# Kernel tuning notes

Measured on AMD Instinct MI355X. Metric: run time of the kernel, lower is better.

Reference implementation:

```python
import jax, jax.numpy as jnp
import numpy as np

B, K, D, LS, NL = 32, 64, 256, 128, 2


def _xavier(key, shape):
    # torch xavier_uniform for Linear weight [out, in]
    fan_out, fan_in = shape[-2], shape[-1]
    lim = float(np.sqrt(6.0 / (fan_in + fan_out)))
    return jax.random.uniform(key, shape, jnp.float32, -lim, lim)


def setup_inputs():
    key = jax.random.key(0)
    ks = jax.random.split(key, 32)
    inp = {
        "X": jax.random.normal(ks[0], (B, K, D), jnp.float32),
        # per-layer stacked params [NL, ...]
        "k_w": _xavier(ks[1], (NL, D, D)),
        "q_w": _xavier(ks[2], (NL, D, D)),
        "rv_w1": _xavier(ks[3], (NL, D, 2 * D)),
        "rv_b1": jnp.zeros((NL, D), jnp.float32),
        "rv_w2": _xavier(ks[4], (NL, D, D)),
        "rv_b2": jnp.zeros((NL, D), jnp.float32),
        "ln_g": jnp.ones((NL, D), jnp.float32),
        "ln_b": jnp.zeros((NL, D), jnp.float32),
        "mlp_w1": _xavier(ks[5], (NL, D, D)),
        "mlp_b1": jnp.zeros((NL, D), jnp.float32),
        "mlp_w2": _xavier(ks[6], (NL, D, D)),
        "mlp_b2": jnp.zeros((NL, D), jnp.float32),
        "proj_w": _xavier(ks[7], (LS, D)),
        "proj_b": jnp.zeros((LS,), jnp.float32),
        "mu_w": _xavier(ks[8], (LS, LS)),
        "mu_b": jnp.zeros((LS,), jnp.float32),
        "sp_w": _xavier(ks[9], (LS, LS)),
        "sp_b": jnp.zeros((LS,), jnp.float32),
    }
    return inp


def _gelu(x):
    return jax.nn.gelu(x, approximate=False)


def _layernorm(x, g, b, eps=1e-5):
    m = jnp.mean(x, axis=-1, keepdims=True)
    v = jnp.mean((x - m) ** 2, axis=-1, keepdims=True)
    return (x - m) / jnp.sqrt(v + eps) * g + b


def _block(x, kw, qw, rw1, rb1, rw2, rb2, lg, lb, mw1, mb1, mw2, mb2):
    scale = D ** (-0.5)
    x_orig = x
    # pairwise difference r[b,i,j,:] = x[b,i]-x[b,j]
    r = x[:, :, None, :] - x[:, None, :, :]                      # [B,K,K,D]
    xi = jnp.broadcast_to(x[:, :, None, :], (B, K, K, D))
    cat = jnp.concatenate([xi, r], axis=-1)                      # [B,K,K,2D]
    v = _gelu(jnp.einsum('bijc,dc->bijd', cat, rw1) + rb1)
    v = jnp.einsum('bijd,ed->bije', v, rw2) + rb2                # [B,K,K,D]
    k = jnp.einsum('bid,ed->bie', x, kw)
    q = jnp.einsum('bid,ed->bie', x, qw) * scale
    attn = jax.nn.softmax(jnp.einsum('bid,bjd->bij', q, k), axis=2)
    agg = jnp.einsum('bij,bijd->bid', attn, v)
    h = _layernorm(x_orig + agg, lg, lb)
    h = jnp.einsum('bid,ed->bie', _gelu(jnp.einsum('bid,ed->bie', h, mw1) + mb1), mw2) + mb2
    return x_orig + h


def reference(X, k_w, q_w, rv_w1, rv_b1, rv_w2, rv_b2, ln_g, ln_b,
              mlp_w1, mlp_b1, mlp_w2, mlp_b2, proj_w, proj_b,
              mu_w, mu_b, sp_w, sp_b):
    x = X
    for i in range(NL):
        x = _block(x, k_w[i], q_w[i], rv_w1[i], rv_b1[i], rv_w2[i], rv_b2[i],
                   ln_g[i], ln_b[i], mlp_w1[i], mlp_b1[i], mlp_w2[i], mlp_b2[i])
    s = jnp.sum(x, axis=1)                                        # [B,D]
    h = _gelu(s @ proj_w.T + proj_b)                              # [B,LS]
    mu = h @ mu_w.T + mu_b
    scale = jax.nn.softplus(h @ sp_w.T + sp_b)
    return (mu, scale)
```

## Files before the change

### kernel.cpp

```cpp
#include <hip/hip_runtime.h>
#include <hip/hip_bf16.h>

#define NL 2

using bf16 = __hip_bfloat16;
typedef short bf16x8 __attribute__((ext_vector_type(8)));
typedef float f32x4 __attribute__((ext_vector_type(4)));

__device__ __forceinline__ float bfu(unsigned short u) { return __uint_as_float(((unsigned)u) << 16); }

__device__ __forceinline__ unsigned short bfr(float v) {
  unsigned u = __float_as_uint(v);
  u += 0x7FFFu + ((u >> 16) & 1u);
  return (unsigned short)(u >> 16);
}

__device__ __forceinline__ float gelu_s(float x) {
  float e = __expf(-1.702f * x);
  return x * __builtin_amdgcn_rcpf(1.0f + e);
}

__device__ __forceinline__ float gelu_e(float x) {
  return 0.5f * x * (1.0f + erff(x * 0.7071067811865475f));
}

__device__ __forceinline__ float load_f(const void* p, int i, int fl) {
  if (fl) return bfu(((const unsigned short*)p)[i]);
  return ((const float*)p)[i];
}

__device__ __forceinline__ int block_detect(const void* X) {
  __shared__ int bad_s;
  if (threadIdx.x == 0) bad_s = 0;
  __syncthreads();
  if (threadIdx.x < 256) {
    const float v = bfu(((const unsigned short*)X)[threadIdx.x]);
    if (!(fabsf(v) < 1e6f)) atomicOr(&bad_s, 1);
  }
  __syncthreads();
  return bad_s ? 0 : 1;
}

__device__ __forceinline__ void stage_split4(unsigned short (&aF)[2][4096], int row, int d0, float4 v) {
  ushort4 h, lo;
  h.x = bfr(v.x); h.y = bfr(v.y); h.z = bfr(v.z); h.w = bfr(v.w);
  lo.x = bfr(v.x - bfu(h.x)); lo.y = bfr(v.y - bfu(h.y));
  lo.z = bfr(v.z - bfu(h.z)); lo.w = bfr(v.w - bfu(h.w));
  const int kt = d0 >> 5, lane = row | (((d0 >> 3) & 3) << 4), j = d0 & 7;
  *(ushort4*)&aF[0][kt*512 + lane*8 + j] = h;
  *(ushort4*)&aF[1][kt*512 + lane*8 + j] = lo;
}

__global__ __launch_bounds__(256) void prep_kernel(
    const void* __restrict__ X, const void* __restrict__ kw, const void* __restrict__ qw,
    const void* __restrict__ rw1, const void* __restrict__ rw2, const void* __restrict__ mw1,
    const void* __restrict__ mw2, const void* __restrict__ pw, const void* __restrict__ muw,
    const void* __restrict__ spw,
    const void* __restrict__ rb1, const void* __restrict__ rb2, const void* __restrict__ lng,
    const void* __restrict__ lnb, const void* __restrict__ mb1, const void* __restrict__ mb2,
    const void* __restrict__ pb, const void* __restrict__ mub, const void* __restrict__ spb,
    unsigned short* __restrict__ wfb, unsigned short* __restrict__ w3b,
    float* __restrict__ wh, float* __restrict__ bc)
{
  __shared__ __align__(16) char psm[65536];
  const int fl = block_detect(X);
  const int t = threadIdx.x;
  int blk = blockIdx.x;

  if (blk < 16) {
    unsigned short* ls = (unsigned short*)psm;
    unsigned* lsu = (unsigned*)psm;
    const int l = blk >> 3, kt = blk & 7;
    if (fl) {
      #pragma unroll
      for (int s = 0; s < 4; ++s) {
        const unsigned* sp = (const unsigned*)((s == 0) ? kw : (s == 1) ? qw : rw1);
        const int rstr = (s < 2) ? 128 : 256;
        const int coff = ((s == 3) ? 128 : 0) + kt*16;
        for (int i = t; i < 4096; i += 256) {
          const int e = i >> 4, d2 = i & 15;
          lsu[s*4096 + i] = sp[(l*256 + e)*rstr + coff + d2];
        }
      }
    } else {
      #pragma unroll
      for (int s = 0; s < 4; ++s) {
        const float* sp = (const float*)((s == 0) ? kw : (s == 1) ? qw : rw1);
        const int rstr = (s < 2) ? 256 : 512;
        const int coff = ((s == 3) ? 256 : 0) + kt*32;
        for (int i = t; i < 4096; i += 256) {
          const int e = i >> 4, d2 = i & 15;
          const float f0 = sp[(l*256 + e)*rstr + coff + d2*2];
          const float f1 = sp[(l*256 + e)*rstr + coff + d2*2 + 1];
          lsu[s*4096 + i] = (unsigned)bfr(f0) | ((unsigned)bfr(f1) << 16);
        }
      }
    }
    __syncthreads();
    unsigned* outp = (unsigned*)wfb + (l*8 + kt)*16384;
    for (int f2 = t; f2 < 16384; f2 += 256) {
      const int j2 = f2 & 3, lane = (f2 >> 2) & 63, ntg = f2 >> 8;
      const int seg = ntg >> 4;
      const int e = (ntg & 15)*16 + (lane & 15);
      const int dl = ((lane >> 4) & 3)*8 + j2*2;
      unsigned short r0 = ls[seg*8192 + e*32 + dl];
      unsigned short r1 = ls[seg*8192 + e*32 + dl + 1];
      if (seg == 1) { r0 = bfr(bfu(r0)*0.0625f); r1 = bfr(bfu(r1)*0.0625f); }
      else if (seg == 2) {
        const unsigned short w0 = ls[3*8192 + e*32 + dl];
        const unsigned short w1 = ls[3*8192 + e*32 + dl + 1];
        r0 = bfr(bfu(r0) + bfu(w0)); r1 = bfr(bfu(r1) + bfu(w1));
      }
      outp[f2] = (unsigned)r0 | ((unsigned)r1 << 16);
    }
    return;
  }
  blk -= 16;
  if (blk < 48) {
    unsigned short* ls = (unsigned short*)psm;
    unsigned* lsu = (unsigned*)psm;
    const int l3 = blk >> 3, kt = blk & 7;
    const int l = l3 / 3, gm = l3 % 3;
    const void* src = (gm == 0) ? rw2 : (gm == 1) ? mw1 : mw2;
    if (fl) {
      const unsigned* sp = (const unsigned*)src;
      for (int i = t; i < 4096; i += 256) {
        const int e = i >> 4, d2 = i & 15;
        lsu[i] = sp[(l*256 + e)*128 + kt*16 + d2];
      }
    } else {
      const float* sp = (const float*)src;
      for (int i = t; i < 4096; i += 256) {
        const int e = i >> 4, d2 = i & 15;
        const float f0 = sp[(l*256 + e)*256 + kt*32 + d2*2];
        const float f1 = sp[(l*256 + e)*256 + kt*32 + d2*2 + 1];
        lsu[i] = (unsigned)bfr(f0) | ((unsigned)bfr(f1) << 16);
      }
    }
    __syncthreads();
    unsigned* outp = (unsigned*)w3b + (l3*8 + kt)*4096;
    for (int f2 = t; f2 < 4096; f2 += 256) {
      const int j2 = f2 & 3, lane = (f2 >> 2) & 63, nt = f2 >> 8;
      const int e = nt*16 + (lane & 15);
      const int dl = ((lane >> 4) & 3)*8 + j2*2;
      outp[f2] = (unsigned)ls[e*32 + dl] | ((unsigned)ls[e*32 + dl + 1] << 16);
    }
    return;
  }
  blk -= 48;
  if (blk < 24) {
    float* lsf = (float*)psm;
    if (blk < 8) {
      const int l0 = blk*16;
      if (fl) {
        const unsigned* sp = (const unsigned*)pw;
        for (int i = t; i < 2048; i += 256) {
          const int ll = i >> 7, d2 = i & 127;
          const unsigned u = sp[(l0 + ll)*128 + d2];
          lsf[ll*256 + d2*2]     = __uint_as_float(u << 16);
          lsf[ll*256 + d2*2 + 1] = __uint_as_float(u & 0xffff0000u);
        }
      } else {
        const float* sp = (const float*)pw;
        for (int i = t; i < 4096; i += 256) {
          const int ll = i >> 8, d = i & 255;
          lsf[ll*256 + d] = sp[(l0 + ll)*256 + d];
        }
      }
      __syncthreads();
      for (int i = t; i < 4096; i += 256) {
        const int d = i >> 4, ll = i & 15;
        wh[d*128 + l0 + ll] = lsf[ll*256 + d];
      }
    } else {
      const int grp = blk - 8;
      const int isSp = grp >> 3;
      const int l0 = (grp & 7)*16;
      const void* src = isSp ? spw : muw;
      const int off = isSp ? 49152 : 32768;
      if (fl) {
        const unsigned* sp = (const unsigned*)src;
        for (int i = t; i < 1024; i += 256) {
          const int ll = i >> 6, c2 = i & 63;
          const unsigned u = sp[(l0 + ll)*64 + c2];
          lsf[ll*128 + c2*2]     = __uint_as_float(u << 16);
          lsf[ll*128 + c2*2 + 1] = __uint_as_float(u & 0xffff0000u);
        }
      } else {
        const float* sp = (const float*)src;
        for (int i = t; i < 2048; i += 256) {
          const int ll = i >> 7, c = i & 127;
          lsf[ll*128 + c] = sp[(l0 + ll)*128 + c];
        }
      }
      __syncthreads();
      for (int i = t; i < 2048; i += 256) {
        const int c = i >> 4, ll = i & 15;
        wh[off + c*128 + l0 + ll] = lsf[ll*128 + c];
      }
    }
    return;
  }
  for (int i = t; i < 3456; i += 256) {
    const void* src; int off;
    if (i < 512)       { src = rb1; off = i; }
    else if (i < 1024) { src = rb2; off = i - 512; }
    else if (i < 1536) { src = lng; off = i - 1024; }
    else if (i < 2048) { src = lnb; off = i - 1536; }
    else if (i < 2560) { src = mb1; off = i - 2048; }
    else if (i < 3072) { src = mb2; off = i - 2560; }
    else if (i < 3200) { src = pb;  off = i - 3072; }
    else if (i < 3328) { src = mub; off = i - 3200; }
    else               { src = spb; off = i - 3328; }
    bc[i] = load_f(src, off, fl);
  }
}

template<bool SPLIT>
__device__ __forceinline__ void k1_body(
    const unsigned short (&aF)[2][4096],
    const unsigned short* __restrict__ wfb, const float* __restrict__ bc,
    float* __restrict__ kq, float* __restrict__ Pf, unsigned* __restrict__ Qpk,
    int l, int row0, int t)
{
  const int w = t >> 6, l64 = t & 63;
  const int col = l64 & 15, quad = l64 >> 4;
  f32x4 acc[8];
  #pragma unroll
  for (int i = 0; i < 8; ++i) acc[i] = (f32x4){0.f, 0.f, 0.f, 0.f};
  for (int kt = 0; kt < 8; ++kt) {
    const bf16x8 ah = *(const bf16x8*)&aF[0][kt*512 + l64*8];
    bf16x8 al;
    if (SPLIT) al = *(const bf16x8*)&aF[1][kt*512 + l64*8];
    #pragma unroll
    for (int i = 0; i < 8; ++i) {
      const int ntg = w*8 + i;
      const bf16x8 b = *(const bf16x8*)&wfb[((l*8 + kt)*64 + ntg)*512 + l64*8];
      acc[i] = __builtin_amdgcn_mfma_f32_16x16x32_bf16(ah, b, acc[i], 0, 0, 0);
      if (SPLIT) acc[i] = __builtin_amdgcn_mfma_f32_16x16x32_bf16(al, b, acc[i], 0, 0, 0);
    }
  }
  #pragma unroll
  for (int i = 0; i < 8; ++i) {
    const int ntg = w*8 + i;
    if (ntg < 32) {
      const int n = ntg*16 + col;
      #pragma unroll
      for (int r = 0; r < 4; ++r)
        kq[(size_t)(row0 + quad*4 + r)*512 + n] = acc[i][r];
    } else if (ntg < 48) {
      const int c = (ntg - 32)*16 + col;
      const float bias = bc[l*256 + c];
      #pragma unroll
      for (int r = 0; r < 4; ++r)
        Pf[(size_t)(row0 + quad*4 + r)*256 + c] = acc[i][r] + bias;
    } else {
      #pragma unroll
      for (int r = 0; r < 4; ++r) {
        const float v = acc[i][r];
        const float pv = __shfl_xor(v, 1, 64);
        if (!(col & 1)) {
          const unsigned uu = (unsigned)bfr(v) | ((unsigned)bfr(pv) << 16);
          Qpk[(size_t)(row0 + quad*4 + r)*128 + (ntg - 48)*8 + (col >> 1)] = uu;
        }
      }
    }
  }
}

__global__ __launch_bounds__(512) void k1l0(
    const void* __restrict__ X, const unsigned short* __restrict__ wfb,
    const float* __restrict__ bc, float* __restrict__ kq, float* __restrict__ Pf,
    unsigned* __restrict__ Qpk)
{
  const int fl = block_detect(X);
  __shared__ __align__(16) unsigned short aF[2][4096];
  const int t = threadIdx.x;
  const int row0 = blockIdx.x * 16;
  if (fl) {
    const int c = t;
    const int row = c >> 5, d0 = (c & 31) * 8;
    const uint4 u = *(const uint4*)((const unsigned*)X + (size_t)(row0 + row)*128 + (c & 31)*4);
    const int kt = d0 >> 5, lane = row | (((d0 >> 3) & 3) << 4);
    *(uint4*)&aF[0][kt*512 + lane*8] = u;
  } else {
    for (int i = t; i < 1024; i += 512) {
      const int row = i >> 6, d0 = (i & 63) * 4;
      const float4 v = *(const float4*)((const float*)X + (size_t)(row0 + row)*256 + d0);
      stage_split4(aF, row, d0, v);
    }
  }
  __syncthreads();
  if (fl) k1_body<false>(aF, wfb, bc, kq, Pf, Qpk, 0, row0, t);
  else    k1_body<true >(aF, wfb, bc, kq, Pf, Qpk, 0, row0, t);
}

__global__ __launch_bounds__(256) void k23_attn(
    const float* __restrict__ kq, const float* __restrict__ Pf,
    const unsigned* __restrict__ Qpk, float* __restrict__ g)
{
  __shared__ unsigned qls[8192];
  __shared__ float qs[4][256];
  __shared__ float sc[4][64];
  __shared__ float als[4][64];
  const int t = threadIdx.x;
  const int b = (int)blockIdx.x >> 4, rq = (int)blockIdx.x & 15;
  const int base = b << 6, i0 = rq * 4;
  {
    const float4* src = (const float4*)(Qpk + (size_t)base*128);
    float4* dst = (float4*)qls;
    for (int i = t; i < 2048; i += 256) dst[i] = src[i];
  }
  for (int i = t; i < 1024; i += 256)
    qs[i >> 8][i & 255] = kq[(size_t)(base + i0 + (i >> 8))*512 + 256 + (i & 255)];
  __syncthreads();

  {
    const int w = t >> 6, lane = t & 63;
    const int jl = lane & 15, part = lane >> 4;
    const int j = w*16 + jl;
    const float* krow = kq + (size_t)(base + j)*512 + part*64;
    float s0 = 0.f, s1 = 0.f, s2 = 0.f, s3 = 0.f;
    for (int dd = 0; dd < 64; dd += 4) {
      const float4 kv = *(const float4*)&krow[dd];
      const float4 q0 = *(const float4*)&qs[0][part*64 + dd];
      const float4 q1 = *(const float4*)&qs[1][part*64 + dd];
      const float4 q2 = *(const float4*)&qs[2][part*64 + dd];
      const float4 q3 = *(const float4*)&qs[3][part*64 + dd];
      s0 = fmaf(kv.x, q0.x, s0); s0 = fmaf(kv.y, q0.y, s0); s0 = fmaf(kv.z, q0.z, s0); s0 = fmaf(kv.w, q0.w, s0);
      s1 = fmaf(kv.x, q1.x, s1); s1 = fmaf(kv.y, q1.y, s1); s1 = fmaf(kv.z, q1.z, s1); s1 = fmaf(kv.w, q1.w, s1);
      s2 = fmaf(kv.x, q2.x, s2); s2 = fmaf(kv.y, q2.y, s2); s2 = fmaf(kv.z, q2.z, s2); s2 = fmaf(kv.w, q2.w, s2);
      s3 = fmaf(kv.x, q3.x, s3); s3 = fmaf(kv.y, q3.y, s3); s3 = fmaf(kv.z, q3.z, s3); s3 = fmaf(kv.w, q3.w, s3);
    }
    s0 += __shfl_xor(s0, 16, 64); s0 += __shfl_xor(s0, 32, 64);
    s1 += __shfl_xor(s1, 16, 64); s1 += __shfl_xor(s1, 32, 64);
    s2 += __shfl_xor(s2, 16, 64); s2 += __shfl_xor(s2, 32, 64);
    s3 += __shfl_xor(s3, 16, 64); s3 += __shfl_xor(s3, 32, 64);
    if (part == 0) { sc[0][j] = s0; sc[1][j] = s1; sc[2][j] = s2; sc[3][j] = s3; }
  }
  __syncthreads();
  {
    const int row = t >> 6, j = t & 63;
    float s = sc[row][j];
    float m = s;
    #pragma unroll
    for (int off = 32; off; off >>= 1) m = fmaxf(m, __shfl_xor(m, off, 64));
    const float e = __expf(s - m);
    float ss = e;
    #pragma unroll
    for (int off = 32; off; off >>= 1) ss += __shfl_xor(ss, off, 64);
    als[row][j] = e / ss;
  }
  __syncthreads();

  const int rg = t >> 7, cp = t & 127;
  const int r0 = base + i0 + rg*2;
  const float2 P0 = *(const float2*)&Pf[(size_t)r0*256 + cp*2];
  const float2 P1 = *(const float2*)&Pf[(size_t)(r0 + 1)*256 + cp*2];
  const float A00 = -1.702f * P0.x, A01 = -1.702f * P0.y;
  const float A10 = -1.702f * P1.x, A11 = -1.702f * P1.y;
  const float* a0p = &als[rg*2][0];
  const float* a1p = &als[rg*2 + 1][0];
  float acc00 = 0.f, acc01 = 0.f, acc10 = 0.f, acc11 = 0.f;
  #pragma unroll 4
  for (int j = 0; j < 64; ++j) {
    const unsigned u = qls[j*128 + cp];
    const float w0 = a0p[j], w1 = a1p[j];
    const float q0 = __uint_as_float(u << 16);
    const float q1 = __uint_as_float(u & 0xffff0000u);
    const float s00 = __builtin_amdgcn_rcpf(1.f + __expf(fmaf(1.702f, q0, A00)));
    const float s01 = __builtin_amdgcn_rcpf(1.f + __expf(fmaf(1.702f, q1, A01)));
    const float s10 = __builtin_amdgcn_rcpf(1.f + __expf(fmaf(1.702f, q0, A10)));
    const float s11 = __builtin_amdgcn_rcpf(1.f + __expf(fmaf(1.702f, q1, A11)));
    acc00 = fmaf(w0 * (P0.x - q0), s00, acc00);
    acc01 = fmaf(w0 * (P0.y - q1), s01, acc01);
    acc10 = fmaf(w1 * (P1.x - q0), s10, acc10);
    acc11 = fmaf(w1 * (P1.y - q1), s11, acc11);
  }
  *(float2*)&g[(size_t)r0*256 + cp*2]       = make_float2(acc00, acc01);
  *(float2*)&g[(size_t)(r0 + 1)*256 + cp*2] = make_float2(acc10, acc11);
}

__device__ __forceinline__ void k4_gemm8(
    f32x4 acc[2], const unsigned short (&aF)[2][4096],
    const unsigned short* __restrict__ wg, int w, int l64)
{
  acc[0] = (f32x4){0.f, 0.f, 0.f, 0.f};
  acc[1] = (f32x4){0.f, 0.f, 0.f, 0.f};
  for (int kt = 0; kt < 8; ++kt) {
    const bf16x8 ah = *(const bf16x8*)&aF[0][kt*512 + l64*8];
    const bf16x8 al = *(const bf16x8*)&aF[1][kt*512 + l64*8];
    #pragma unroll
    for (int nt = 0; nt < 2; ++nt) {
      const bf16x8 b = *(const bf16x8*)&wg[((kt*16 + (w*2 + nt))*64 + l64)*8];
      acc[nt] = __builtin_amdgcn_mfma_f32_16x16x32_bf16(ah, b, acc[nt], 0, 0, 0);
      acc[nt] = __builtin_amdgcn_mfma_f32_16x16x32_bf16(al, b, acc[nt], 0, 0, 0);
    }
  }
}

template<bool ADAPT, bool TAIL>
__device__ __forceinline__ void k4_core(
    const float* __restrict__ g, const void* __restrict__ xin, int fl,
    float* __restrict__ xout, const unsigned short* __restrict__ wg,
    const float* __restrict__ bc, int l, int row0, int t,
    unsigned short (&aF)[2][4096], float* bufB, float (&mv)[16][2])
{
  const int w = t >> 6, l64 = t & 63;
  const int col = l64 & 15, quad = l64 >> 4;
  const float* rb2c = bc + 512  + l*256;
  const float* lngc = bc + 1024 + l*256;
  const float* lnbc = bc + 1536 + l*256;
  const float* mb1c = bc + 2048 + l*256;
  const float* mb2c = bc + 2560 + l*256;

  for (int i = t; i < 1024; i += 512) {
    const int row = i >> 6, d0 = (i & 63) * 4;
    stage_split4(aF, row, d0, *(const float4*)&g[(size_t)(row0 + row)*256 + d0]);
  }
  if (ADAPT && fl) {
    for (int c = t; c < 2048; c += 512) {
      const int row = c >> 7, dp = c & 127;
      const unsigned u = ((const unsigned*)xin)[(size_t)(row0 + row)*128 + dp];
      bufB[row*260 + dp*2]     = __uint_as_float(u << 16);
      bufB[row*260 + dp*2 + 1] = __uint_as_float(u & 0xffff0000u);
    }
  } else {
    for (int c = t; c < 1024; c += 512) {
      const int row = c >> 6, d0 = (c & 63) * 4;
      *(float4*)&bufB[row*260 + d0] = *(const float4*)((const float*)xin + (size_t)(row0 + row)*256 + d0);
    }
  }
  __syncthreads();
  float xtr[2][4];
  #pragma unroll
  for (int nt = 0; nt < 2; ++nt) {
    const int cn = (w*2 + nt)*16 + col;
    #pragma unroll
    for (int r = 0; r < 4; ++r) xtr[nt][r] = bufB[(quad*4 + r)*260 + cn];
  }
  __syncthreads();

  f32x4 acc[2];
  k4_gemm8(acc, aF, wg, w, l64);
  #pragma unroll
  for (int nt = 0; nt < 2; ++nt) {
    const int cn = (w*2 + nt)*16 + col;
    #pragma unroll
    for (int r = 0; r < 4; ++r)
      bufB[(quad*4 + r)*260 + cn] = acc[nt][r] + rb2c[cn] + xtr[nt][r];
  }
  __syncthreads();
  {
    const int row = t >> 5, part = t & 31;
    float s = 0.f, s2 = 0.f;
    #pragma unroll
    for (int kk = 0; kk < 8; ++kk) {
      const float v = bufB[row*260 + part + kk*32];
      s += v; s2 = fmaf(v, v, s2);
    }
    #pragma unroll
    for (int off = 16; off; off >>= 1) {
      s  += __shfl_xor(s, off, 32);
      s2 += __shfl_xor(s2, off, 32);
    }
    if (part == 0) {
      const float mu = s * (1.f/256.f);
      mv[row][0] = mu;
      mv[row][1] = rsqrtf(fmaf(-mu, mu, s2 * (1.f/256.f)) + 1e-5f);
    }
  }
  __syncthreads();
  for (int i = t; i < 1024; i += 512) {
    const int row = i >> 6, d0 = (i & 63) * 4;
    float4 v = *(const float4*)&bufB[row*260 + d0];
    const float m = mv[row][0], iv = mv[row][1];
    v.x = (v.x - m)*iv*lngc[d0]   + lnbc[d0];
    v.y = (v.y - m)*iv*lngc[d0+1] + lnbc[d0+1];
    v.z = (v.z - m)*iv*lngc[d0+2] + lnbc[d0+2];
    v.w = (v.w - m)*iv*lngc[d0+3] + lnbc[d0+3];
    stage_split4(aF, row, d0, v);
  }
  __syncthreads();
  k4_gemm8(acc, aF, wg + 65536, w, l64);
  #pragma unroll
  for (int nt = 0; nt < 2; ++nt) {
    const int cn = (w*2 + nt)*16 + col;
    #pragma unroll
    for (int r = 0; r < 4; ++r)
      bufB[(quad*4 + r)*260 + cn] = gelu_e(acc[nt][r] + mb1c[cn]);
  }
  __syncthreads();
  for (int i = t; i < 1024; i += 512) {
    const int row = i >> 6, d0 = (i & 63) * 4;
    stage_split4(aF, row, d0, *(const float4*)&bufB[row*260 + d0]);
  }
  __syncthreads();
  k4_gemm8(acc, aF, wg + 2*65536, w, l64);
  if (TAIL) {
    #pragma unroll
    for (int nt = 0; nt < 2; ++nt) {
      const int cn = (w*2 + nt)*16 + col;
      #pragma unroll
      for (int r = 0; r < 4; ++r)
        bufB[(quad*4 + r)*260 + cn] = acc[nt][r] + mb2c[cn] + xtr[nt][r];
    }
    __syncthreads();
    for (int i = t; i < 1024; i += 512) {
      const int row = i >> 6, d0 = (i & 63) * 4;
      const float4 v = *(const float4*)&bufB[row*260 + d0];
      *(float4*)&xout[(size_t)(row0 + row)*256 + d0] = v;
      stage_split4(aF, row, d0, v);
    }
    __syncthreads();
  } else {
    #pragma unroll
    for (int nt = 0; nt < 2; ++nt) {
      const int cn = (w*2 + nt)*16 + col;
      #pragma unroll
      for (int r = 0; r < 4; ++r)
        xout[(size_t)(row0 + quad*4 + r)*256 + cn] = acc[nt][r] + mb2c[cn] + xtr[nt][r];
    }
  }
}

__global__ __launch_bounds__(512) void k41_mix_kq(
    const float* __restrict__ g, const unsigned short* __restrict__ w3b,
    const unsigned short* __restrict__ wfb, const float* __restrict__ bc,
    const void* __restrict__ X, float* __restrict__ x,
    float* __restrict__ kq, float* __restrict__ Pf, unsigned* __restrict__ Qpk)
{
  const int fl = block_detect(X);
  __shared__ __align__(16) unsigned short aF[2][4096];
  __shared__ float bufB[16*260];
  __shared__ float mv[16][2];
  const int t = threadIdx.x;
  const int row0 = blockIdx.x * 16;
  k4_core<true, true>(g, X, fl, x, w3b, bc, 0, row0, t, aF, bufB, mv);
  k1_body<true>(aF, wfb, bc, kq, Pf, Qpk, 1, row0, t);
}

__global__ __launch_bounds__(512) void k4_fin(
    const float* __restrict__ g, const unsigned short* __restrict__ w3b,
    const float* __restrict__ bc, float* __restrict__ x)
{
  __shared__ __align__(16) unsigned short aF[2][4096];
  __shared__ float bufB[16*260];
  __shared__ float mv[16][2];
  const int t = threadIdx.x;
  const int row0 = blockIdx.x * 16;
  k4_core<false, false>(g, x, 0, x, w3b + 3*65536, bc, 1, row0, t, aF, bufB, mv);
}

__global__ __launch_bounds__(256) void k5_head(
    const float* __restrict__ x, const float* __restrict__ wh,
    const float* __restrict__ bc, const void* __restrict__ X,
    void* __restrict__ out)
{
  const int fl = block_detect(X);
  __shared__ float ss[256];
  __shared__ float hh[128];
  const int b = blockIdx.x, t = threadIdx.x;
  float s = 0.f;
  for (int i = 0; i < 64; ++i) s += x[(size_t)((b << 6) + i)*256 + t];
  ss[t] = s;
  __syncthreads();
  if (t < 128) {
    float acc = bc[3072 + t];
    const float* projT = wh;
    for (int d = 0; d < 256; ++d) acc = fmaf(ss[d], projT[d*128 + t], acc);
    hh[t] = gelu_e(acc);
  }
  __syncthreads();
  float v; int oidx;
  if (t < 128) {
    float acc = bc[3200 + t];
    const float* muT = wh + 32768;
    for (int c = 0; c < 128; ++c) acc = fmaf(hh[c], muT[c*128 + t], acc);
    v = acc; oidx = b*128 + t;
  } else {
    const int u = t - 128;
    float acc = bc[3328 + u];
    const float* spT = wh + 49152;
    for (int c = 0; c < 128; ++c) acc = fmaf(hh[c], spT[c*128 + u], acc);
    v = (acc > 20.f) ? acc : log1pf(__expf(acc));
    oidx = 4096 + b*128 + u;
  }
  if (fl) ((bf16*)out)[oidx] = __float2bfloat16(v);
  else    ((float*)out)[oidx] = v;
}

extern "C" void kernel_launch(void* const* d_in, const int* in_sizes, int n_in,
                              void* d_out, int out_size, void* d_ws, size_t ws_size,
                              hipStream_t stream)
{
  (void)in_sizes; (void)n_in; (void)out_size; (void)ws_size;
  float* ws    = (float*)d_ws;
  float* x     = ws + 16;
  float* kq    = x + 524288;
  float* Pf    = kq + 1048576;
  unsigned* Qpk = (unsigned*)(Pf + 524288);
  float* g     = (float*)(Qpk + 262144);
  unsigned short* wfb = (unsigned short*)(g + 524288);
  unsigned short* w3b = wfb + 524288;
  float* wh    = (float*)(w3b + 393216);
  float* bc    = wh + 65536;

  prep_kernel<<<dim3(89), dim3(256), 0, stream>>>(
      d_in[0], d_in[1], d_in[2], d_in[3], d_in[5], d_in[9], d_in[11],
      d_in[13], d_in[15], d_in[17],
      d_in[4], d_in[6], d_in[7], d_in[8], d_in[10], d_in[12],
      d_in[14], d_in[16], d_in[18],
      wfb, w3b, wh, bc);
  k1l0<<<dim3(128), dim3(512), 0, stream>>>(d_in[0], wfb, bc, kq, Pf, Qpk);
  k23_attn<<<dim3(512), dim3(256), 0, stream>>>(kq, Pf, Qpk, g);
  k41_mix_kq<<<dim3(128), dim3(512), 0, stream>>>(g, w3b, wfb, bc, d_in[0], x, kq, Pf, Qpk);
  k23_attn<<<dim3(512), dim3(256), 0, stream>>>(kq, Pf, Qpk, g);
  k4_fin<<<dim3(128), dim3(512), 0, stream>>>(g, w3b, bc, x);
  k5_head<<<dim3(32), dim3(256), 0, stream>>>(x, wh, bc, d_in[0], (void*)d_out);
}
```

Before: 213.8 us.

## Split work across more blocks in GEMM, attention and MLP kernels

Raises grid sizes so the launches cover all compute units. The first projection GEMM is split across four column-group blocks, and attention handles two query rows per block with Qpk read straight from global memory instead of being staged in LDS. The fused MLP+KQ kernel now uses two blocks per row tile, each recomputing the MLP and producing half the KQ columns, and the final MLP works on 8-row tiles. In exchange it duplicates MLP work, wastes half of each 16-row MFMA tile, and rereads weights and Qpk from global memory more often.

```diff
diff --git a/kernel.cpp b/kernel.cpp
--- a/kernel.cpp
+++ b/kernel.cpp
@@ -1,7 +1,6 @@
 #include <hip/hip_runtime.h>
 #include <hip/hip_bf16.h>
 
-#define NL 2
 
 using bf16 = __hip_bfloat16;
 typedef short bf16x8 __attribute__((ext_vector_type(8)));
@@ -13,11 +12,6 @@
   unsigned u = __float_as_uint(v);
   u += 0x7FFFu + ((u >> 16) & 1u);
   return (unsigned short)(u >> 16);
-}
-
-__device__ __forceinline__ float gelu_s(float x) {
-  float e = __expf(-1.702f * x);
-  return x * __builtin_amdgcn_rcpf(1.0f + e);
 }
 
 __device__ __forceinline__ float gelu_e(float x) {
@@ -173,9 +167,9 @@
         wh[d*128 + l0 + ll] = lsf[ll*256 + d];
       }
     } else {
-      const int grp = blk - 8;
-      const int isSp = grp >> 3;
-      const int l0 = (grp & 7)*16;
+      const int grp2 = blk - 8;
+      const int isSp = grp2 >> 3;
+      const int l0 = (grp2 & 7)*16;
       const void* src = isSp ? spw : muw;
       const int off = isSp ? 49152 : 32768;
       if (fl) {
@@ -216,33 +210,33 @@
   }
 }
 
-template<bool SPLIT>
+template<bool SPLIT, int NTG>
 __device__ __forceinline__ void k1_body(
     const unsigned short (&aF)[2][4096],
     const unsigned short* __restrict__ wfb, const float* __restrict__ bc,
     float* __restrict__ kq, float* __restrict__ Pf, unsigned* __restrict__ Qpk,
-    int l, int row0, int t)
+    int l, int row0, int ntg0, int t)
 {
   const int w = t >> 6, l64 = t & 63;
   const int col = l64 & 15, quad = l64 >> 4;
-  f32x4 acc[8];
+  f32x4 acc[NTG];
   #pragma unroll
-  for (int i = 0; i < 8; ++i) acc[i] = (f32x4){0.f, 0.f, 0.f, 0.f};
+  for (int i = 0; i < NTG; ++i) acc[i] = (f32x4){0.f, 0.f, 0.f, 0.f};
   for (int kt = 0; kt < 8; ++kt) {
     const bf16x8 ah = *(const bf16x8*)&aF[0][kt*512 + l64*8];
     bf16x8 al;
     if (SPLIT) al = *(const bf16x8*)&aF[1][kt*512 + l64*8];
     #pragma unroll
-    for (int i = 0; i < 8; ++i) {
-      const int ntg = w*8 + i;
+    for (int i = 0; i < NTG; ++i) {
+      const int ntg = ntg0 + w*NTG + i;
       const bf16x8 b = *(const bf16x8*)&wfb[((l*8 + kt)*64 + ntg)*512 + l64*8];
       acc[i] = __builtin_amdgcn_mfma_f32_16x16x32_bf16(ah, b, acc[i], 0, 0, 0);
       if (SPLIT) acc[i] = __builtin_amdgcn_mfma_f32_16x16x32_bf16(al, b, acc[i], 0, 0, 0);
     }
   }
   #pragma unroll
-  for (int i = 0; i < 8; ++i) {
-    const int ntg = w*8 + i;
+  for (int i = 0; i < NTG; ++i) {
+    const int ntg = ntg0 + w*NTG + i;
     if (ntg < 32) {
       const int n = ntg*16 + col;
       #pragma unroll
@@ -268,7 +262,7 @@
   }
 }
 
-__global__ __launch_bounds__(512) void k1l0(
+__global__ __launch_bounds__(256) void k1l0(
     const void* __restrict__ X, const unsigned short* __restrict__ wfb,
     const float* __restrict__ bc, float* __restrict__ kq, float* __restrict__ Pf,
     unsigned* __restrict__ Qpk)
@@ -276,72 +270,64 @@
   const int fl = block_detect(X);
   __shared__ __align__(16) unsigned short aF[2][4096];
   const int t = threadIdx.x;
-  const int row0 = blockIdx.x * 16;
+  const int mb = (int)blockIdx.x >> 2, nb4 = (int)blockIdx.x & 3;
+  const int row0 = mb * 16, ntg0 = nb4 * 16;
   if (fl) {
-    const int c = t;
-    const int row = c >> 5, d0 = (c & 31) * 8;
-    const uint4 u = *(const uint4*)((const unsigned*)X + (size_t)(row0 + row)*128 + (c & 31)*4);
-    const int kt = d0 >> 5, lane = row | (((d0 >> 3) & 3) << 4);
-    *(uint4*)&aF[0][kt*512 + lane*8] = u;
+    for (int i = t; i < 512; i += 256) {
+      const int row = i >> 5, d0 = (i & 31) * 8;
+      const uint4 u = *(const uint4*)((const unsigned*)X + (size_t)(row0 + row)*128 + (i & 31)*4);
+      const int kt = d0 >> 5, lane = row | (((d0 >> 3) & 3) << 4);
+      *(uint4*)&aF[0][kt*512 + lane*8] = u;
+    }
   } else {
-    for (int i = t; i < 1024; i += 512) {
+    for (int i = t; i < 1024; i += 256) {
       const int row = i >> 6, d0 = (i & 63) * 4;
-      const float4 v = *(const float4*)((const float*)X + (size_t)(row0 + row)*256 + d0);
-      stage_split4(aF, row, d0, v);
-    }
-  }
-  __syncthreads();
-  if (fl) k1_body<false>(aF, wfb, bc, kq, Pf, Qpk, 0, row0, t);
-  else    k1_body<true >(aF, wfb, bc, kq, Pf, Qpk, 0, row0, t);
+      stage_split4(aF, row, d0, *(const float4*)((const float*)X + (size_t)(row0 + row)*256 + d0));
+    }
+  }
+  __syncthreads();
+  if (fl) k1_body<false, 4>(aF, wfb, bc, kq, Pf, Qpk, 0, row0, ntg0, t);
+  else    k1_body<true,  4>(aF, wfb, bc, kq, Pf, Qpk, 0, row0, ntg0, t);
 }
 
 __global__ __launch_bounds__(256) void k23_attn(
     const float* __restrict__ kq, const float* __restrict__ Pf,
     const unsigned* __restrict__ Qpk, float* __restrict__ g)
 {
-  __shared__ unsigned qls[8192];
-  __shared__ float qs[4][256];
-  __shared__ float sc[4][64];
-  __shared__ float als[4][64];
+  __shared__ float qs[2][256];
+  __shared__ float scp[2][64];
+  __shared__ float als[2][64];
   const int t = threadIdx.x;
-  const int b = (int)blockIdx.x >> 4, rq = (int)blockIdx.x & 15;
-  const int base = b << 6, i0 = rq * 4;
-  {
-    const float4* src = (const float4*)(Qpk + (size_t)base*128);
-    float4* dst = (float4*)qls;
-    for (int i = t; i < 2048; i += 256) dst[i] = src[i];
-  }
-  for (int i = t; i < 1024; i += 256)
+  const int b = (int)blockIdx.x >> 5, ip = (int)blockIdx.x & 31;
+  const int base = b << 6, i0 = ip * 2;
+  for (int i = t; i < 512; i += 256)
     qs[i >> 8][i & 255] = kq[(size_t)(base + i0 + (i >> 8))*512 + 256 + (i & 255)];
   __syncthreads();
-
   {
     const int w = t >> 6, lane = t & 63;
     const int jl = lane & 15, part = lane >> 4;
     const int j = w*16 + jl;
     const float* krow = kq + (size_t)(base + j)*512 + part*64;
-    float s0 = 0.f, s1 = 0.f, s2 = 0.f, s3 = 0.f;
+    const float* q0p = &qs[0][part*64];
+    const float* q1p = &qs[1][part*64];
+    float s0 = 0.f, s1 = 0.f;
     for (int dd = 0; dd < 64; dd += 4) {
       const float4 kv = *(const float4*)&krow[dd];
-      const float4 q0 = *(const float4*)&qs[0][part*64 + dd];
-      const float4 q1 = *(const float4*)&qs[1][part*64 + dd];
-      const float4 q2 = *(const float4*)&qs[2][part*64 + dd];
-      const float4 q3 = *(const float4*)&qs[3][part*64 + dd];
-      s0 = fmaf(kv.x, q0.x, s0); s0 = fmaf(kv.y, q0.y, s0); s0 = fmaf(kv.z, q0.z, s0); s0 = fmaf(kv.w, q0.w, s0);
-      s1 = fmaf(kv.x, q1.x, s1); s1 = fmaf(kv.y, q1.y, s1); s1 = fmaf(kv.z, q1.z, s1); s1 = fmaf(kv.w, q1.w, s1);
-      s2 = fmaf(kv.x, q2.x, s2); s2 = fmaf(kv.y, q2.y, s2); s2 = fmaf(kv.z, q2.z, s2); s2 = fmaf(kv.w, q2.w, s2);
-      s3 = fmaf(kv.x, q3.x, s3); s3 = fmaf(kv.y, q3.y, s3); s3 = fmaf(kv.z, q3.z, s3); s3 = fmaf(kv.w, q3.w, s3);
+      const float4 q0 = *(const float4*)&q0p[dd];
+      const float4 q1 = *(const float4*)&q1p[dd];
+      s0 = fmaf(kv.x, q0.x, s0); s0 = fmaf(kv.y, q0.y, s0);
+      s0 = fmaf(kv.z, q0.z, s0); s0 = fmaf(kv.w, q0.w, s0);
+      s1 = fmaf(kv.x, q1.x, s1); s1 = fmaf(kv.y, q1.y, s1);
+      s1 = fmaf(kv.z, q1.z, s1); s1 = fmaf(kv.w, q1.w, s1);
     }
     s0 += __shfl_xor(s0, 16, 64); s0 += __shfl_xor(s0, 32, 64);
     s1 += __shfl_xor(s1, 16, 64); s1 += __shfl_xor(s1, 32, 64);
-    s2 += __shfl_xor(s2, 16, 64); s2 += __shfl_xor(s2, 32, 64);
-    s3 += __shfl_xor(s3, 16, 64); s3 += __shfl_xor(s3, 32, 64);
-    if (part == 0) { sc[0][j] = s0; sc[1][j] = s1; sc[2][j] = s2; sc[3][j] = s3; }
-  }
-  __syncthreads();
-  {
+    if (part == 0) { scp[0][j] = s0; scp[1][j] = s1; }
+  }
+  __syncthreads();
+  if (t < 128) {
     const int row = t >> 6, j = t & 63;
-    float s = sc[row][j];
+    float s = scp[row][j];
     float m = s;
     #pragma unroll
     for (int off = 32; off; off >>= 1) m = fmaxf(m, __shfl_xor(m, off, 64));
@@ -352,33 +338,25 @@
     als[row][j] = e / ss;
   }
   __syncthreads();
-
   const int rg = t >> 7, cp = t & 127;
-  const int r0 = base + i0 + rg*2;
-  const float2 P0 = *(const float2*)&Pf[(size_t)r0*256 + cp*2];
-  const float2 P1 = *(const float2*)&Pf[(size_t)(r0 + 1)*256 + cp*2];
-  const float A00 = -1.702f * P0.x, A01 = -1.702f * P0.y;
-  const float A10 = -1.702f * P1.x, A11 = -1.702f * P1.y;
-  const float* a0p = &als[rg*2][0];
-  const float* a1p = &als[rg*2 + 1][0];
-  float acc00 = 0.f, acc01 = 0.f, acc10 = 0.f, acc11 = 0.f;
-  #pragma unroll 4
+  const int r = base + i0 + rg;
+  const float2 P = *(const float2*)&Pf[(size_t)r*256 + cp*2];
+  const float A0 = -1.702f * P.x, A1 = -1.702f * P.y;
+  const float* ap = &als[rg][0];
+  const unsigned* qp = Qpk + (size_t)base*128 + cp;
+  float acc0 = 0.f, acc1 = 0.f;
+  #pragma unroll 8
   for (int j = 0; j < 64; ++j) {
-    const unsigned u = qls[j*128 + cp];
-    const float w0 = a0p[j], w1 = a1p[j];
+    const unsigned u = qp[j*128];
+    const float wgt = ap[j];
     const float q0 = __uint_as_float(u << 16);
     const float q1 = __uint_as_float(u & 0xffff0000u);
-    const float s00 = __builtin_amdgcn_rcpf(1.f + __expf(fmaf(1.702f, q0, A00)));
-    const float s01 = __builtin_amdgcn_rcpf(1.f + __expf(fmaf(1.702f, q1, A01)));
-    const float s10 = __builtin_amdgcn_rcpf(1.f + __expf(fmaf(1.702f, q0, A10)));
-    const float s11 = __builtin_amdgcn_rcpf(1.f + __expf(fmaf(1.702f, q1, A11)));
-    acc00 = fmaf(w0 * (P0.x - q0), s00, acc00);
-    acc01 = fmaf(w0 * (P0.y - q1), s01, acc01);
-    acc10 = fmaf(w1 * (P1.x - q0), s10, acc10);
-    acc11 = fmaf(w1 * (P1.y - q1), s11, acc11);
-  }
-  *(float2*)&g[(size_t)r0*256 + cp*2]       = make_float2(acc00, acc01);
-  *(float2*)&g[(size_t)(r0 + 1)*256 + cp*2] = make_float2(acc10, acc11);
+    const float s0 = __builtin_amdgcn_rcpf(1.f + __expf(fmaf(1.702f, q0, A0)));
+    const float s1 = __builtin_amdgcn_rcpf(1.f + __expf(fmaf(1.702f, q1, A1)));
+    acc0 = fmaf(wgt * (P.x - q0), s0, acc0);
+    acc1 = fmaf(wgt * (P.y - q1), s1, acc1);
+  }
+  *(float2*)&g[(size_t)r*256 + cp*2] = make_float2(acc0, acc1);
 }
 
 __device__ __forceinline__ void k4_gemm8(
@@ -399,11 +377,11 @@
   }
 }
 
-template<bool ADAPT, bool TAIL>
+template<bool ADAPT, bool TAIL, int NR>
 __device__ __forceinline__ void k4_core(
     const float* __restrict__ g, const void* __restrict__ xin, int fl,
     float* __restrict__ xout, const unsigned short* __restrict__ wg,
-    const float* __restrict__ bc, int l, int row0, int t,
+    const float* __restrict__ bc, int l, int row0, int t, bool writeX,
     unsigned short (&aF)[2][4096], float* bufB, float (&mv)[16][2])
 {
   const int w = t >> 6, l64 = t & 63;
@@ -414,19 +392,19 @@
   const float* mb1c = bc + 2048 + l*256;
   const float* mb2c = bc + 2560 + l*256;
 
-  for (int i = t; i < 1024; i += 512) {
+  for (int i = t; i < NR*64; i += 512) {
     const int row = i >> 6, d0 = (i & 63) * 4;
     stage_split4(aF, row, d0, *(const float4*)&g[(size_t)(row0 + row)*256 + d0]);
   }
   if (ADAPT && fl) {
-    for (int c = t; c < 2048; c += 512) {
+    for (int c = t; c < NR*128; c += 512) {
       const int row = c >> 7, dp = c & 127;
       const unsigned u = ((const unsigned*)xin)[(size_t)(row0 + row)*128 + dp];
       bufB[row*260 + dp*2]     = __uint_as_float(u << 16);
       bufB[row*260 + dp*2 + 1] = __uint_as_float(u & 0xffff0000u);
     }
   } else {
-    for (int c = t; c < 1024; c += 512) {
+    for (int c = t; c < NR*64; c += 512) {
       const int row = c >> 6, d0 = (c & 63) * 4;
       *(float4*)&bufB[row*260 + d0] = *(const float4*)((const float*)xin + (size_t)(row0 + row)*256 + d0);
     }
@@ -453,25 +431,27 @@
   __syncthreads();
   {
     const int row = t >> 5, part = t & 31;
-    float s = 0.f, s2 = 0.f;
-    #pragma unroll
-    for (int kk = 0; kk < 8; ++kk) {
-      const float v = bufB[row*260 + part + kk*32];
-      s += v; s2 = fmaf(v, v, s2);
-    }
-    #pragma unroll
-    for (int off = 16; off; off >>= 1) {
-      s  += __shfl_xor(s, off, 32);
-      s2 += __shfl_xor(s2, off, 32);
-    }
-    if (part == 0) {
-      const float mu = s * (1.f/256.f);
-      mv[row][0] = mu;
-      mv[row][1] = rsqrtf(fmaf(-mu, mu, s2 * (1.f/256.f)) + 1e-5f);
-    }
-  }
-  __syncthreads();
-  for (int i = t; i < 1024; i += 512) {
+    if (row < NR) {
+      float s = 0.f, s2 = 0.f;
+      #pragma unroll
+      for (int kk = 0; kk < 8; ++kk) {
+        const float v = bufB[row*260 + part + kk*32];
+        s += v; s2 = fmaf(v, v, s2);
+      }
+      #pragma unroll
+      for (int off = 16; off; off >>= 1) {
+        s  += __shfl_xor(s, off, 32);
+        s2 += __shfl_xor(s2, off, 32);
+      }
+      if (part == 0) {
+        const float mu = s * (1.f/256.f);
+        mv[row][0] = mu;
+        mv[row][1] = rsqrtf(fmaf(-mu, mu, s2 * (1.f/256.f)) + 1e-5f);
+      }
+    }
+  }
+  __syncthreads();
+  for (int i = t; i < NR*64; i += 512) {
     const int row = i >> 6, d0 = (i & 63) * 4;
     float4 v = *(const float4*)&bufB[row*260 + d0];
     const float m = mv[row][0], iv = mv[row][1];
@@ -488,10 +468,11 @@
     const int cn = (w*2 + nt)*16 + col;
     #pragma unroll
     for (int r = 0; r < 4; ++r)
-      bufB[(quad*4 + r)*260 + cn] = gelu_e(acc[nt][r] + mb1c[cn]);
-  }
-  __syncthreads();
-  for (int i = t; i < 1024; i += 512) {
+      if (quad*4 + r < NR)
+        bufB[(quad*4 + r)*260 + cn] = gelu_e(acc[nt][r] + mb1c[cn]);
+  }
+  __syncthreads();
+  for (int i = t; i < NR*64; i += 512) {
     const int row = i >> 6, d0 = (i & 63) * 4;
     stage_split4(aF, row, d0, *(const float4*)&bufB[row*260 + d0]);
   }
@@ -506,10 +487,10 @@
         bufB[(quad*4 + r)*260 + cn] = acc[nt][r] + mb2c[cn] + xtr[nt][r];
     }
     __syncthreads();
-    for (int i = t; i < 1024; i += 512) {
+    for (int i = t; i < NR*64; i += 512) {
       const int row = i >> 6, d0 = (i & 63) * 4;
       const float4 v = *(const float4*)&bufB[row*260 + d0];
-      *(float4*)&xout[(size_t)(row0 + row)*256 + d0] = v;
+      if (writeX) *(float4*)&xout[(size_t)(row0 + row)*256 + d0] = v;
       stage_split4(aF, row, d0, v);
     }
     __syncthreads();
@@ -519,7 +500,8 @@
       const int cn = (w*2 + nt)*16 + col;
       #pragma unroll
       for (int r = 0; r < 4; ++r)
-        xout[(size_t)(row0 + quad*4 + r)*256 + cn] = acc[nt][r] + mb2c[cn] + xtr[nt][r];
+        if (quad*4 + r < NR)
+          xout[(size_t)(row0 + quad*4 + r)*256 + cn] = acc[nt][r] + mb2c[cn] + xtr[nt][r];
     }
   }
 }
@@ -535,9 +517,10 @@
   __shared__ float bufB[16*260];
   __shared__ float mv[16][2];
   const int t = threadIdx.x;
-  const int row0 = blockIdx.x * 16;
-  k4_core<true, true>(g, X, fl, x, w3b, bc, 0, row0, t, aF, bufB, mv);
-  k1_body<true>(aF, wfb, bc, kq, Pf, Qpk, 1, row0, t);
+  const int rb = (int)blockIdx.x >> 1, parity = (int)blockIdx.x & 1;
+  const int row0 = rb * 16;
+  k4_core<true, true, 16>(g, X, fl, x, w3b, bc, 0, row0, t, parity == 0, aF, bufB, mv);
+  k1_body<true, 4>(aF, wfb, bc, kq, Pf, Qpk, 1, row0, parity*32, t);
 }
 
 __global__ __launch_bounds__(512) void k4_fin(
@@ -548,8 +531,8 @@
   __shared__ float bufB[16*260];
   __shared__ float mv[16][2];
   const int t = threadIdx.x;
-  const int row0 = blockIdx.x * 16;
-  k4_core<false, false>(g, x, 0, x, w3b + 3*65536, bc, 1, row0, t, aF, bufB, mv);
+  const int row0 = blockIdx.x * 8;
+  k4_core<false, false, 8>(g, x, 0, x, w3b + 3*65536, bc, 1, row0, t, true, aF, bufB, mv);
 }
 
 __global__ __launch_bounds__(256) void k5_head(
@@ -612,10 +595,10 @@
       d_in[4], d_in[6], d_in[7], d_in[8], d_in[10], d_in[12],
       d_in[14], d_in[16], d_in[18],
       wfb, w3b, wh, bc);
-  k1l0<<<dim3(128), dim3(512), 0, stream>>>(d_in[0], wfb, bc, kq, Pf, Qpk);
-  k23_attn<<<dim3(512), dim3(256), 0, stream>>>(kq, Pf, Qpk, g);
-  k41_mix_kq<<<dim3(128), dim3(512), 0, stream>>>(g, w3b, wfb, bc, d_in[0], x, kq, Pf, Qpk);
-  k23_attn<<<dim3(512), dim3(256), 0, stream>>>(kq, Pf, Qpk, g);
-  k4_fin<<<dim3(128), dim3(512), 0, stream>>>(g, w3b, bc, x);
+  k1l0<<<dim3(512), dim3(256), 0, stream>>>(d_in[0], wfb, bc, kq, Pf, Qpk);
+  k23_attn<<<dim3(1024), dim3(256), 0, stream>>>(kq, Pf, Qpk, g);
+  k41_mix_kq<<<dim3(256), dim3(512), 0, stream>>>(g, w3b, wfb, bc, d_in[0], x, kq, Pf, Qpk);
+  k23_attn<<<dim3(1024), dim3(256), 0, stream>>>(kq, Pf, Qpk, g);
+  k4_fin<<<dim3(256), dim3(512), 0, stream>>>(g, w3b, bc, x);
   k5_head<<<dim3(32), dim3(256), 0, stream>>>(x, wh, bc, d_in[0], (void*)d_out);
 }
```

After: 208.5 us (median of 2 runs). 2.5% less time.
